# Kernel optimization log

Measured on AMD Instinct MI355X. Metric: run time of the kernel, lower is better.

The kernel has to match this reference:

```python
import jax, jax.numpy as jnp
import numpy as np

B, N, NODE_DIM, HID, HEAD = 32, 1024, 14, 64, 128
EDGE_PROB = 0.01


def setup_inputs() -> dict:
    key = jax.random.key(0)
    ks = jax.random.split(key, 12)
    x = jax.random.normal(ks[0], (B, N, NODE_DIM), dtype=jnp.float32)
    # sparse binary adjacency with self-loops (matches eye + edge scatter)
    adj = (jax.random.uniform(ks[1], (B, N, N)) < EDGE_PROB).astype(jnp.float32)
    adjacency = jnp.maximum(adj, jnp.eye(N, dtype=jnp.float32)[None])
    def lin(k, din, dout):
        kw, kb = jax.random.split(k)
        w = jax.random.normal(kw, (din, dout), dtype=jnp.float32) / np.sqrt(din)
        b = jnp.zeros((dout,), dtype=jnp.float32)
        return w, b
    W1, b1 = lin(ks[2], NODE_DIM, HID)
    W2, b2 = lin(ks[3], HID, HID)
    W3, b3 = lin(ks[4], HID, HID)
    Wf1, bf1 = lin(ks[5], HID, HEAD)
    Wf2, bf2 = lin(ks[6], HEAD, 1)
    return {"x": x, "adjacency": adjacency, "W1": W1, "b1": b1, "W2": W2,
            "b2": b2, "W3": W3, "b3": b3, "Wf1": Wf1, "bf1": bf1,
            "Wf2": Wf2, "bf2": bf2}


def _dense_graph_conv(x, norm_adj, W, b):
    # (D^-1/2 A D^-1/2) @ x, then linear
    return jnp.einsum('bnm,bmd->bnd', norm_adj, x) @ W + b


def reference(x, adjacency, W1, b1, W2, b2, W3, b3, Wf1, bf1, Wf2, bf2):
    degree = adjacency.sum(axis=-1)                      # [B,N]
    d_inv_sqrt = jnp.clip(degree, 1.0, None) ** -0.5
    norm_adj = d_inv_sqrt[..., :, None] * adjacency * d_inv_sqrt[..., None, :]
    h = jax.nn.relu(_dense_graph_conv(x, norm_adj, W1, b1))
    h = jax.nn.relu(_dense_graph_conv(h, norm_adj, W2, b2))
    h = jax.nn.relu(_dense_graph_conv(h, norm_adj, W3, b3))
    pooled = h.mean(axis=1)                              # [B,HID]
    return jax.nn.relu(pooled @ Wf1 + bf1) @ Wf2 + bf2   # [B,1]
```

## Files before the change

kernel.cpp:

```cpp
#include <hip/hip_runtime.h>
#include <math.h>

#define NN 1024
#define HID 64
#define HEADD 128
#define NODE_DIM 14
#define BATCH 32
#define CAP 64
#define ROWS (BATCH * NN)
#define RPW 8

__device__ __forceinline__ int swz4(int blk, int wv) {
    int x = blk & 7, q = blk >> 3;
    int batch = x + 8 * (q >> 8);
    return batch * NN + ((q & 255) << 2) + wv;
}
__device__ __forceinline__ int swz32(int blk, int wv) {
    int x = blk & 7, q = blk >> 3;
    int batch = x + 8 * (q >> 5);
    return batch * NN + ((q & 31) << 5) + wv * RPW;
}

__device__ __forceinline__ float rl_f(float v, int k) {
    return __int_as_float(__builtin_amdgcn_readlane(__float_as_int(v), k));
}

__global__ __launch_bounds__(256) void k_build(const float* __restrict__ adj,
                                               const float* __restrict__ x,
                                               const float* __restrict__ W1,
                                               unsigned short* __restrict__ csr,
                                               int* __restrict__ nnz_g,
                                               float* __restrict__ dinv,
                                               float* __restrict__ g1,
                                               float* __restrict__ pooled) {
    __shared__ float sW1[NODE_DIM * HID];
    for (int i = threadIdx.x; i < NODE_DIM * HID; i += 256) sW1[i] = W1[i];
    if (blockIdx.x < 8) pooled[blockIdx.x * 256 + threadIdx.x] = 0.f;
    int wv = threadIdx.x >> 6, lane = threadIdx.x & 63;
    int row = swz4(blockIdx.x, wv);
    const float4* rp = reinterpret_cast<const float4*>(adj + (size_t)row * NN);
    unsigned long long lt = ((unsigned long long)1 << lane) - 1;
    int base = 0;
#pragma unroll
    for (int j = 0; j < 4; ++j) {
        float4 v = rp[lane + 64 * j];
        float vv[4] = {v.x, v.y, v.z, v.w};
#pragma unroll
        for (int k = 0; k < 4; ++k) {
            unsigned long long mk = __ballot(vv[k] != 0.0f);
            if (mk) {
                if (vv[k] != 0.0f) {
                    int pos = base + __popcll(mk & lt);
                    if (pos < CAP)
                        csr[row * CAP + pos] = (unsigned short)((lane + 64 * j) * 4 + k);
                }
                base += __popcll(mk);
            }
        }
    }
    if (lane == 0) {
        nnz_g[row] = base < CAP ? base : CAP;
        dinv[row] = 1.0f / sqrtf((float)(base < 1 ? 1 : base));
    }
    __syncthreads();
    float acc = 0.f;
    const float* xr = x + (size_t)row * NODE_DIM;
#pragma unroll
    for (int d = 0; d < NODE_DIM; ++d) acc += xr[d] * sW1[d * HID + lane];
    g1[(size_t)row * HID + lane] = acc;
}

__device__ __forceinline__ void spmm8(const float* __restrict__ g_in,
                                      int bbase, const int n[RPW],
                                      const int idx[RPW], const float dv[RPW],
                                      int lane, float acc[RPW]) {
    int nmax = 0;
#pragma unroll
    for (int r = 0; r < RPW; ++r) { acc[r] = 0.f; nmax = n[r] > nmax ? n[r] : nmax; }
    for (int k = 0; k < nmax; ++k) {
        float w[RPW], v[RPW];
#pragma unroll
        for (int r = 0; r < RPW; ++r) {
            int j = __builtin_amdgcn_readlane(idx[r], k);
            w[r] = rl_f(dv[r], k);
            v[r] = g_in[(bbase + j) * HID + lane];
        }
#pragma unroll
        for (int r = 0; r < RPW; ++r) acc[r] += w[r] * v[r];
    }
}

__global__ __launch_bounds__(256, 4) void k_layer(const float* __restrict__ g_in,
                                                  const unsigned short* __restrict__ csr,
                                                  const int* __restrict__ nnz_g,
                                                  const float* __restrict__ dinv,
                                                  const float* __restrict__ bias,
                                                  const float* __restrict__ W,
                                                  float* __restrict__ g_out) {
    __shared__ float sW[HID * HID];
    for (int i = threadIdx.x; i < HID * HID; i += 256) sW[i] = W[i];
    int wv = threadIdx.x >> 6, lane = threadIdx.x & 63;
    int row0 = swz32(blockIdx.x, wv);
    int bbase = row0 & ~(NN - 1);
    float bb = bias[lane];
    int n[RPW], idx[RPW];
    float dv[RPW];
#pragma unroll
    for (int r = 0; r < RPW; ++r) {
        int row = row0 + r;
        n[r] = __builtin_amdgcn_readfirstlane(nnz_g[row]);
        idx[r] = (lane < n[r]) ? (int)csr[row * CAP + lane] : 0;
        dv[r] = (lane < n[r]) ? dinv[bbase + idx[r]] : 0.f;
    }
    float acc[RPW];
    spmm8(g_in, bbase, n, idx, dv, lane, acc);
    float h[RPW];
#pragma unroll
    for (int r = 0; r < RPW; ++r)
        h[r] = fmaxf(dinv[row0 + r] * acc[r] + bb, 0.f);
    __syncthreads();
    float o[RPW];
#pragma unroll
    for (int r = 0; r < RPW; ++r) o[r] = 0.f;
    for (int d = 0; d < HID; ++d) {
        float w = sW[d * HID + lane];
#pragma unroll
        for (int r = 0; r < RPW; ++r) o[r] += rl_f(h[r], d) * w;
    }
#pragma unroll
    for (int r = 0; r < RPW; ++r)
        g_out[(size_t)(row0 + r) * HID + lane] = o[r];
}

__global__ __launch_bounds__(256, 4) void k_layer3(const float* __restrict__ g_in,
                                                   const unsigned short* __restrict__ csr,
                                                   const int* __restrict__ nnz_g,
                                                   const float* __restrict__ dinv,
                                                   const float* __restrict__ bias,
                                                   float* __restrict__ pooled) {
    __shared__ float sred[4][HID];
    int wv = threadIdx.x >> 6, lane = threadIdx.x & 63;
    int row0 = swz32(blockIdx.x, wv);
    int bbase = row0 & ~(NN - 1);
    float bb = bias[lane];
    int n[RPW], idx[RPW];
    float dv[RPW];
#pragma unroll
    for (int r = 0; r < RPW; ++r) {
        int row = row0 + r;
        n[r] = __builtin_amdgcn_readfirstlane(nnz_g[row]);
        idx[r] = (lane < n[r]) ? (int)csr[row * CAP + lane] : 0;
        dv[r] = (lane < n[r]) ? dinv[bbase + idx[r]] : 0.f;
    }
    float acc[RPW];
    spmm8(g_in, bbase, n, idx, dv, lane, acc);
    float s = 0.f;
#pragma unroll
    for (int r = 0; r < RPW; ++r)
        s += fmaxf(dinv[row0 + r] * acc[r] + bb, 0.f);
    sred[wv][lane] = s;
    __syncthreads();
    if (wv == 0) {
        float tot = sred[0][lane] + sred[1][lane] + sred[2][lane] + sred[3][lane];
        atomicAdd(&pooled[(bbase >> 10) * HID + lane], tot);
    }
}

__global__ __launch_bounds__(128) void k_head(const float* __restrict__ pooled_sum,
                                              const float* __restrict__ Wf1,
                                              const float* __restrict__ bf1,
                                              const float* __restrict__ Wf2,
                                              const float* __restrict__ bf2,
                                              float* __restrict__ out) {
    int b = blockIdx.x, t = threadIdx.x;
    __shared__ float p[HID];
    __shared__ float hid[HEADD];
    if (t < HID) p[t] = pooled_sum[b * HID + t] * (1.0f / NN);
    __syncthreads();
    float acc = bf1[t];
    for (int d = 0; d < HID; ++d) acc += p[d] * Wf1[d * HEADD + t];
    hid[t] = fmaxf(acc, 0.f);
    __syncthreads();
    if (t < 64) {
        float v = hid[t] * Wf2[t] + hid[t + 64] * Wf2[t + 64];
#pragma unroll
        for (int off = 32; off > 0; off >>= 1) v += __shfl_down(v, off, 64);
        if (t == 0) out[b] = v + bf2[0];
    }
}

extern "C" void kernel_launch(void* const* d_in, const int* in_sizes, int n_in,
                              void* d_out, int out_size, void* d_ws, size_t ws_size,
                              hipStream_t stream) {
    const float* x   = (const float*)d_in[0];
    const float* adj = (const float*)d_in[1];
    const float* W1  = (const float*)d_in[2];
    const float* b1  = (const float*)d_in[3];
    const float* W2  = (const float*)d_in[4];
    const float* b2  = (const float*)d_in[5];
    const float* W3  = (const float*)d_in[6];
    const float* b3  = (const float*)d_in[7];
    const float* Wf1 = (const float*)d_in[8];
    const float* bf1 = (const float*)d_in[9];
    const float* Wf2 = (const float*)d_in[10];
    const float* bf2 = (const float*)d_in[11];
    float* out = (float*)d_out;

    char* ws = (char*)d_ws;
    size_t off = 0;
    unsigned short* csr = (unsigned short*)(ws + off); off += (size_t)ROWS * CAP * 2;
    int*   nnz_g  = (int*)(ws + off);   off += (size_t)ROWS * 4;
    float* dinv   = (float*)(ws + off); off += (size_t)ROWS * 4;
    float* pooled = (float*)(ws + off); off += 4096 * 4;
    float* g1     = (float*)(ws + off); off += (size_t)ROWS * HID * 4;
    float* g2     = (float*)(ws + off); off += (size_t)ROWS * HID * 4;
    float* g3     = (float*)(ws + off);

    k_build <<<ROWS / 4, 256, 0, stream>>>(adj, x, W1, csr, nnz_g, dinv, g1, pooled);
    k_layer <<<ROWS / 32, 256, 0, stream>>>(g1, csr, nnz_g, dinv, b1, W2, g2);
    k_layer <<<ROWS / 32, 256, 0, stream>>>(g2, csr, nnz_g, dinv, b2, W3, g3);
    k_layer3<<<ROWS / 32, 256, 0, stream>>>(g3, csr, nnz_g, dinv, b3, pooled);
    k_head  <<<BATCH, 128, 0, stream>>>(pooled, Wf1, bf1, Wf2, bf2, out);
}
```

Before: 300.0 us.

## Fuse head into last layer via ticket, widen CSR, use LDS for dense matmul

Several changes land together. The head MLP is folded into the last layer kernel: an atomic ticket picks the final block, which then computes the head for all batches, so one launch disappears. CSR indices widen from u16 to int, and the h@W product now reads h from shared memory as float4 instead of broadcasting with readlane. Feature buffers are ping-ponged and the occupancy hint is dropped. The costs are twice the CSR bytes, a large shared allocation in the last kernel that may cut occupancy, and a serial head computed by a single block.

```diff
diff --git a/kernel.cpp b/kernel.cpp
--- a/kernel.cpp
+++ b/kernel.cpp
@@ -9,6 +9,7 @@
 #define CAP 64
 #define ROWS (BATCH * NN)
 #define RPW 8
+#define LAYER_BLOCKS (ROWS / 32)
 
 __device__ __forceinline__ int swz4(int blk, int wv) {
     int x = blk & 7, q = blk >> 3;
@@ -28,14 +29,16 @@
 __global__ __launch_bounds__(256) void k_build(const float* __restrict__ adj,
                                                const float* __restrict__ x,
                                                const float* __restrict__ W1,
-                                               unsigned short* __restrict__ csr,
+                                               int* __restrict__ csr,
                                                int* __restrict__ nnz_g,
                                                float* __restrict__ dinv,
                                                float* __restrict__ g1,
-                                               float* __restrict__ pooled) {
+                                               float* __restrict__ pooled,
+                                               int* __restrict__ ticket) {
     __shared__ float sW1[NODE_DIM * HID];
     for (int i = threadIdx.x; i < NODE_DIM * HID; i += 256) sW1[i] = W1[i];
     if (blockIdx.x < 8) pooled[blockIdx.x * 256 + threadIdx.x] = 0.f;
+    if (blockIdx.x == 8 && threadIdx.x == 0) ticket[0] = 0;
     int wv = threadIdx.x >> 6, lane = threadIdx.x & 63;
     int row = swz4(blockIdx.x, wv);
     const float4* rp = reinterpret_cast<const float4*>(adj + (size_t)row * NN);
@@ -51,8 +54,7 @@
             if (mk) {
                 if (vv[k] != 0.0f) {
                     int pos = base + __popcll(mk & lt);
-                    if (pos < CAP)
-                        csr[row * CAP + pos] = (unsigned short)((lane + 64 * j) * 4 + k);
+                    if (pos < CAP) csr[row * CAP + pos] = (lane + 64 * j) * 4 + k;
                 }
                 base += __popcll(mk);
             }
@@ -90,70 +92,89 @@
     }
 }
 
-__global__ __launch_bounds__(256, 4) void k_layer(const float* __restrict__ g_in,
-                                                  const unsigned short* __restrict__ csr,
-                                                  const int* __restrict__ nnz_g,
-                                                  const float* __restrict__ dinv,
-                                                  const float* __restrict__ bias,
-                                                  const float* __restrict__ W,
-                                                  float* __restrict__ g_out) {
+__device__ __forceinline__ void gather_rows(const float* __restrict__ g_in,
+                                            const int* __restrict__ csr,
+                                            const int* __restrict__ nnz_g,
+                                            const float* __restrict__ dinv,
+                                            int row0, int bbase, int lane,
+                                            float acc[RPW]) {
+    int n[RPW], idx[RPW];
+    float dv[RPW];
+#pragma unroll
+    for (int r = 0; r < RPW; ++r) {
+        int row = row0 + r;
+        n[r] = __builtin_amdgcn_readfirstlane(nnz_g[row]);
+        idx[r] = (lane < n[r]) ? csr[row * CAP + lane] : 0;
+        dv[r] = (lane < n[r]) ? dinv[bbase + idx[r]] : 0.f;
+    }
+    spmm8(g_in, bbase, n, idx, dv, lane, acc);
+}
+
+__global__ __launch_bounds__(256) void k_layer(const float* __restrict__ g_in,
+                                               const int* __restrict__ csr,
+                                               const int* __restrict__ nnz_g,
+                                               const float* __restrict__ dinv,
+                                               const float* __restrict__ bias,
+                                               const float* __restrict__ W,
+                                               float* __restrict__ g_out) {
     __shared__ float sW[HID * HID];
+    __shared__ float sh[4][RPW][HID];
     for (int i = threadIdx.x; i < HID * HID; i += 256) sW[i] = W[i];
+    __syncthreads();
     int wv = threadIdx.x >> 6, lane = threadIdx.x & 63;
     int row0 = swz32(blockIdx.x, wv);
     int bbase = row0 & ~(NN - 1);
     float bb = bias[lane];
-    int n[RPW], idx[RPW];
-    float dv[RPW];
-#pragma unroll
-    for (int r = 0; r < RPW; ++r) {
-        int row = row0 + r;
-        n[r] = __builtin_amdgcn_readfirstlane(nnz_g[row]);
-        idx[r] = (lane < n[r]) ? (int)csr[row * CAP + lane] : 0;
-        dv[r] = (lane < n[r]) ? dinv[bbase + idx[r]] : 0.f;
-    }
     float acc[RPW];
-    spmm8(g_in, bbase, n, idx, dv, lane, acc);
-    float h[RPW];
+    gather_rows(g_in, csr, nnz_g, dinv, row0, bbase, lane, acc);
 #pragma unroll
     for (int r = 0; r < RPW; ++r)
-        h[r] = fmaxf(dinv[row0 + r] * acc[r] + bb, 0.f);
-    __syncthreads();
+        sh[wv][r][lane] = fmaxf(dinv[row0 + r] * acc[r] + bb, 0.f);
     float o[RPW];
 #pragma unroll
     for (int r = 0; r < RPW; ++r) o[r] = 0.f;
-    for (int d = 0; d < HID; ++d) {
-        float w = sW[d * HID + lane];
-#pragma unroll
-        for (int r = 0; r < RPW; ++r) o[r] += rl_f(h[r], d) * w;
+#pragma unroll
+    for (int dq = 0; dq < HID / 4; ++dq) {
+        float w0 = sW[(dq * 4 + 0) * HID + lane];
+        float w1 = sW[(dq * 4 + 1) * HID + lane];
+        float w2 = sW[(dq * 4 + 2) * HID + lane];
+        float w3 = sW[(dq * 4 + 3) * HID + lane];
+#pragma unroll
+        for (int r = 0; r < RPW; ++r) {
+            float4 hq = *reinterpret_cast<const float4*>(&sh[wv][r][dq * 4]);
+            o[r] += hq.x * w0;
+            o[r] += hq.y * w1;
+            o[r] += hq.z * w2;
+            o[r] += hq.w * w3;
+        }
     }
 #pragma unroll
     for (int r = 0; r < RPW; ++r)
         g_out[(size_t)(row0 + r) * HID + lane] = o[r];
 }
 
-__global__ __launch_bounds__(256, 4) void k_layer3(const float* __restrict__ g_in,
-                                                   const unsigned short* __restrict__ csr,
-                                                   const int* __restrict__ nnz_g,
-                                                   const float* __restrict__ dinv,
-                                                   const float* __restrict__ bias,
-                                                   float* __restrict__ pooled) {
+__global__ __launch_bounds__(256) void k_layer3h(const float* __restrict__ g_in,
+                                                 const int* __restrict__ csr,
+                                                 const int* __restrict__ nnz_g,
+                                                 const float* __restrict__ dinv,
+                                                 const float* __restrict__ bias,
+                                                 float* __restrict__ pooled,
+                                                 int* __restrict__ ticket,
+                                                 const float* __restrict__ Wf1,
+                                                 const float* __restrict__ bf1,
+                                                 const float* __restrict__ Wf2,
+                                                 const float* __restrict__ bf2,
+                                                 float* __restrict__ out) {
     __shared__ float sred[4][HID];
+    __shared__ int s_last;
+    __shared__ float sp[BATCH * HID];
+    __shared__ float shid[BATCH * HEADD];
     int wv = threadIdx.x >> 6, lane = threadIdx.x & 63;
     int row0 = swz32(blockIdx.x, wv);
     int bbase = row0 & ~(NN - 1);
     float bb = bias[lane];
-    int n[RPW], idx[RPW];
-    float dv[RPW];
-#pragma unroll
-    for (int r = 0; r < RPW; ++r) {
-        int row = row0 + r;
-        n[r] = __builtin_amdgcn_readfirstlane(nnz_g[row]);
-        idx[r] = (lane < n[r]) ? (int)csr[row * CAP + lane] : 0;
-        dv[r] = (lane < n[r]) ? dinv[bbase + idx[r]] : 0.f;
-    }
     float acc[RPW];
-    spmm8(g_in, bbase, n, idx, dv, lane, acc);
+    gather_rows(g_in, csr, nnz_g, dinv, row0, bbase, lane, acc);
     float s = 0.f;
 #pragma unroll
     for (int r = 0; r < RPW; ++r)
@@ -164,28 +185,33 @@
         float tot = sred[0][lane] + sred[1][lane] + sred[2][lane] + sred[3][lane];
         atomicAdd(&pooled[(bbase >> 10) * HID + lane], tot);
     }
-}
-
-__global__ __launch_bounds__(128) void k_head(const float* __restrict__ pooled_sum,
-                                              const float* __restrict__ Wf1,
-                                              const float* __restrict__ bf1,
-                                              const float* __restrict__ Wf2,
-                                              const float* __restrict__ bf2,
-                                              float* __restrict__ out) {
-    int b = blockIdx.x, t = threadIdx.x;
-    __shared__ float p[HID];
-    __shared__ float hid[HEADD];
-    if (t < HID) p[t] = pooled_sum[b * HID + t] * (1.0f / NN);
-    __syncthreads();
-    float acc = bf1[t];
-    for (int d = 0; d < HID; ++d) acc += p[d] * Wf1[d * HEADD + t];
-    hid[t] = fmaxf(acc, 0.f);
-    __syncthreads();
-    if (t < 64) {
-        float v = hid[t] * Wf2[t] + hid[t + 64] * Wf2[t + 64];
-#pragma unroll
-        for (int off = 32; off > 0; off >>= 1) v += __shfl_down(v, off, 64);
-        if (t == 0) out[b] = v + bf2[0];
+    __syncthreads();
+    if (threadIdx.x == 0) {
+        __threadfence();
+        int old = atomicAdd(ticket, 1);
+        s_last = (old == LAYER_BLOCKS - 1) ? 1 : 0;
+    }
+    __syncthreads();
+    if (s_last) {
+        __threadfence();
+        int t = threadIdx.x;
+        for (int i = t; i < BATCH * HID; i += 256)
+            sp[i] = atomicAdd(&pooled[i], 0.0f) * (1.0f / NN);
+        __syncthreads();
+        for (int task = t; task < BATCH * HEADD; task += 256) {
+            int b = task >> 7, c = task & (HEADD - 1);
+            float a = bf1[c];
+            for (int d = 0; d < HID; ++d)
+                a += sp[b * HID + d] * Wf1[d * HEADD + c];
+            shid[task] = fmaxf(a, 0.f);
+        }
+        __syncthreads();
+        if (t < BATCH) {
+            float v = 0.f;
+            for (int c = 0; c < HEADD; ++c)
+                v += shid[t * HEADD + c] * Wf2[c];
+            out[t] = v + bf2[0];
+        }
     }
 }
 
@@ -208,17 +234,18 @@
 
     char* ws = (char*)d_ws;
     size_t off = 0;
-    unsigned short* csr = (unsigned short*)(ws + off); off += (size_t)ROWS * CAP * 2;
+    int*   csr    = (int*)(ws + off);   off += (size_t)ROWS * CAP * 4;
     int*   nnz_g  = (int*)(ws + off);   off += (size_t)ROWS * 4;
     float* dinv   = (float*)(ws + off); off += (size_t)ROWS * 4;
     float* pooled = (float*)(ws + off); off += 4096 * 4;
-    float* g1     = (float*)(ws + off); off += (size_t)ROWS * HID * 4;
-    float* g2     = (float*)(ws + off); off += (size_t)ROWS * HID * 4;
-    float* g3     = (float*)(ws + off);
-
-    k_build <<<ROWS / 4, 256, 0, stream>>>(adj, x, W1, csr, nnz_g, dinv, g1, pooled);
-    k_layer <<<ROWS / 32, 256, 0, stream>>>(g1, csr, nnz_g, dinv, b1, W2, g2);
-    k_layer <<<ROWS / 32, 256, 0, stream>>>(g2, csr, nnz_g, dinv, b2, W3, g3);
-    k_layer3<<<ROWS / 32, 256, 0, stream>>>(g3, csr, nnz_g, dinv, b3, pooled);
-    k_head  <<<BATCH, 128, 0, stream>>>(pooled, Wf1, bf1, Wf2, bf2, out);
-}
+    int*   ticket = (int*)(ws + off);   off += 256;
+    float* gA     = (float*)(ws + off); off += (size_t)ROWS * HID * 4;
+    float* gB     = (float*)(ws + off);
+
+    k_build  <<<ROWS / 4, 256, 0, stream>>>(adj, x, W1, csr, nnz_g, dinv, gA,
+                                            pooled, ticket);
+    k_layer  <<<LAYER_BLOCKS, 256, 0, stream>>>(gA, csr, nnz_g, dinv, b1, W2, gB);
+    k_layer  <<<LAYER_BLOCKS, 256, 0, stream>>>(gB, csr, nnz_g, dinv, b2, W3, gA);
+    k_layer3h<<<LAYER_BLOCKS, 256, 0, stream>>>(gA, csr, nnz_g, dinv, b3, pooled,
+                                                ticket, Wf1, bf1, Wf2, bf2, out);
+}
```

Result: slower. 314.8 us (+4.9%).
